# Kernel tuning notes

Measured on AMD Instinct MI355X. Metric: run time of the kernel, lower is better.

The kernel has to match this reference:

```python
import jax, jax.numpy as jnp
import numpy as np

EPS = 1e-5  # BatchNorm eps (torch default)

def _wq(w):
    # W8A16 fake-quant: per-output-channel symmetric int8 quantize + dequantize
    s = jnp.max(jnp.abs(w), axis=tuple(range(1, w.ndim)), keepdims=True) / 127.0
    s = jnp.maximum(s, 1e-8)
    q = jnp.clip(jnp.round(w / s), -128.0, 127.0)
    return q * s

def _conv(x, w, b, pad):
    y = jax.lax.conv_general_dilated(x, _wq(w), (1, 1), [(pad, pad), (pad, pad)],
                                     dimension_numbers=('NCHW', 'OIHW', 'NCHW'))
    return y + b[None, :, None, None]

def _bn(x, g, b, m, v):
    sh = (1, -1, 1, 1) if x.ndim == 4 else (1, -1)
    inv = jax.lax.rsqrt(v + EPS)
    return (x - m.reshape(sh)) * (inv * g).reshape(sh) + b.reshape(sh)

def _pool(x):
    return jax.lax.reduce_window(x, -jnp.inf, jax.lax.max, (1, 1, 2, 2), (1, 1, 2, 2), 'VALID')

def _ht(x):
    return jnp.clip(x, -1.0, 1.0)

def _linear(x, w, b):
    return x @ _wq(w).T + b

def setup_inputs() -> dict:
    key = jax.random.key(0)
    ks = iter(jax.random.split(key, 64))
    def rn(shape, s=0.05):
        return jax.random.normal(next(ks), shape, jnp.float32) * s
    d = {}
    d['x'] = jax.random.normal(next(ks), (1024, 1, 28, 28), jnp.float32)
    convs = [(1, 32, 5), (32, 64, 5), (64, 128, 3), (128, 256, 3), (256, 256, 1)]
    for i, (ci, co, k) in enumerate(convs, 1):
        d[f'w{i}'] = rn((co, ci, k, k), 0.1)
        d[f'b{i}'] = rn((co,))
        d[f'g{i}'] = jnp.ones((co,), jnp.float32)
        d[f'be{i}'] = jnp.zeros((co,), jnp.float32)
        d[f'mu{i}'] = rn((co,))
        d[f'va{i}'] = jax.random.uniform(next(ks), (co,), jnp.float32, 0.5, 1.5)
    fcs = [(2304, 1024), (1024, 512)]
    for i, (fi, fo) in enumerate(fcs, 1):
        d[f'fw{i}'] = rn((fo, fi), 0.05)
        d[f'fb{i}'] = rn((fo,))
        d[f'fg{i}'] = jnp.ones((fo,), jnp.float32)
        d[f'fbe{i}'] = jnp.zeros((fo,), jnp.float32)
        d[f'fmu{i}'] = rn((fo,))
        d[f'fva{i}'] = jax.random.uniform(next(ks), (fo,), jnp.float32, 0.5, 1.5)
    d['fw3'] = rn((10, 512), 0.05)
    d['fb3'] = rn((10,))
    return d

def reference(x, w1, b1, g1, be1, mu1, va1, w2, b2, g2, be2, mu2, va2,
              w3, b3, g3, be3, mu3, va3, w4, b4, g4, be4, mu4, va4,
              w5, b5, g5, be5, mu5, va5,
              fw1, fb1, fg1, fbe1, fmu1, fva1,
              fw2, fb2, fg2, fbe2, fmu2, fva2, fw3, fb3):
    h = _ht(_bn(_conv(x, w1, b1, 2), g1, be1, mu1, va1))                 # [B,32,28,28]
    h = _ht(_bn(_pool(_conv(h, w2, b2, 2)), g2, be2, mu2, va2))          # [B,64,14,14]
    h = _ht(_bn(_pool(_conv(h, w3, b3, 1)), g3, be3, mu3, va3))          # [B,128,7,7]
    h = _ht(_bn(_pool(_conv(h, w4, b4, 1)), g4, be4, mu4, va4))          # [B,256,3,3]
    h = _ht(_bn(_conv(h, w5, b5, 0), g5, be5, mu5, va5))                 # [B,256,3,3]
    h = h.reshape(h.shape[0], -1)                                        # [B,2304]
    h = _ht(_bn(_linear(h, fw1, fb1), fg1, fbe1, fmu1, fva1))            # [B,1024]
    h = _ht(_bn(_linear(h, fw2, fb2), fg2, fbe2, fmu2, fva2))            # [B,512]
    return _linear(h, fw3, fb3)                                          # [B,10]
```

## Files before the change

kernel.cpp:

```cpp
#include <hip/hip_runtime.h>
#include <hip/hip_bf16.h>
#include <math.h>


#define EPS 1e-5f

typedef __attribute__((ext_vector_type(8))) short bf16x8;
typedef __attribute__((ext_vector_type(4))) float f32x4;
typedef __attribute__((ext_vector_type(16))) float f32x16;
typedef __attribute__((ext_vector_type(4))) int i32x4;

__device__ __forceinline__ short f2bf(float f) {
  unsigned u = __builtin_bit_cast(unsigned, f);
  unsigned r = u + 0x7FFFu + ((u >> 16) & 1u);
  return (short)(r >> 16);
}
__device__ __forceinline__ float bf2f(short h) {
  unsigned u = ((unsigned)(unsigned short)h) << 16;
  return __builtin_bit_cast(float, u);
}
__device__ __forceinline__ int swz(int pin, int smask) {
  return (pin ^ (pin >> 2)) & smask;
}

struct QuantArgs {
  const float* w[8];
  float* q[8];
  float* sc[8];
  int cik[8];
  int cum[9];
};

__global__ __launch_bounds__(256) void quant_all(QuantArgs a) {
  int b = blockIdx.x;
  int t = 0;
  while (b >= a.cum[t + 1]) t++;
  int co = b - a.cum[t];
  int cik = a.cik[t];
  const float* src = a.w[t] + (size_t)co * cik;
  float m = 0.f;
  for (int i = threadIdx.x; i < cik; i += 256) m = fmaxf(m, fabsf(src[i]));
  #pragma unroll
  for (int o = 1; o < 64; o <<= 1) m = fmaxf(m, __shfl_xor(m, o));
  __shared__ float red[4];
  __shared__ float ssh;
  if ((threadIdx.x & 63) == 0) red[threadIdx.x >> 6] = m;
  __syncthreads();
  if (threadIdx.x == 0) {
    m = fmaxf(fmaxf(red[0], red[1]), fmaxf(red[2], red[3]));
    float s = fmaxf(m / 127.0f, 1e-8f);
    ssh = s;
    a.sc[t][co] = s;
  }
  __syncthreads();
  float s = ssh;
  float* dst = a.q[t];
  if (dst) {
    float* d = dst + (size_t)co * cik;
    for (int i = threadIdx.x; i < cik; i += 256) {
      float q = rintf(src[i] / s);
      q = fminf(fmaxf(q, -128.f), 127.f);
      d[i] = q * s;
    }
  }
}

__global__ __launch_bounds__(256) void repack_c1(const float* __restrict__ w,
                                                 const float* __restrict__ sc,
                                                 short* __restrict__ dst) {
  int i = blockIdx.x * 256 + threadIdx.x;
  if (i >= 1024) return;
  int oc = i >> 5, t = i & 31;
  float v = 0.f;
  if (t < 25) {
    float s = sc[oc];
    v = fminf(fmaxf(rintf(w[oc * 25 + t] / s), -128.f), 127.f);
  }
  dst[(((oc >> 4) * 4 + (t >> 3)) * 16 + (oc & 15)) * 8 + (t & 7)] = f2bf(v);
}

__global__ __launch_bounds__(256) void repack_frag(const float* __restrict__ w,
                                                   const float* __restrict__ sc,
                                                   short* __restrict__ dst,
                                                   int CO, int CI, int KK, int OCCH) {
  int i = blockIdx.x * 256 + threadIdx.x;
  int total = CO * CI * KK;
  if (i >= total) return;
  int oc = i / (CI * KK);
  int r = i - oc * (CI * KK);
  int ci = r / KK;
  int kk = r - ci * KK;
  float s = sc[oc];
  float q = fminf(fmaxf(rintf(w[i] / s), -128.f), 127.f);
  int NTC = OCCH >> 4;
  int KS = CI >> 5; if (KS == 0) KS = 1;
  int chunk = oc / OCCH;
  int ocl = oc - chunk * OCCH;
  int ntl = ocl >> 4, mr = ocl & 15;
  int ks = ci >> 5, qq = (ci >> 3) & 3, j = ci & 7;
  size_t d = ((((((size_t)(chunk * KK + kk) * NTC + ntl) * KS + ks) * 4 + qq) * 16 + mr)) * 8 + j;
  dst[d] = f2bf(q);
}

__global__ __launch_bounds__(256) void repack_frag32(const float* __restrict__ w,
                                                     const float* __restrict__ sc,
                                                     short* __restrict__ dst,
                                                     int CO, int CI, int KK, int OCCH) {
  int i = blockIdx.x * 256 + threadIdx.x;
  int total = CO * CI * KK;
  if (i >= total) return;
  int oc = i / (CI * KK);
  int r = i - oc * (CI * KK);
  int ci = r / KK;
  int kk = r - ci * KK;
  float s = sc[oc];
  float q = fminf(fmaxf(rintf(w[i] / s), -128.f), 127.f);
  int NT32 = OCCH >> 5;
  int KS16 = CI >> 4;
  int chunk = oc / OCCH;
  int ocl = oc - chunk * OCCH;
  int nt = ocl >> 5, n32 = ocl & 31;
  int ks = ci >> 4, hh = (ci >> 3) & 1, j = ci & 7;
  size_t d = ((((size_t)(chunk * KK + kk) * NT32 + nt) * KS16 + ks) * 64 + hh * 32 + n32) * 8 + j;
  dst[d] = f2bf(q);
}

__global__ __launch_bounds__(256) void repack_fc(const float* __restrict__ w,
                                                 const float* __restrict__ sc,
                                                 short* __restrict__ dst,
                                                 int K, int KC, int total) {
  int i = blockIdx.x * 256 + threadIdx.x;
  if (i >= total) return;
  int n = i / K, k = i - n * K;
  float s = sc[n];
  float q = fminf(fmaxf(rintf(w[i] / s), -128.f), 127.f);
  int nblk = n >> 6, ntl = (n >> 4) & 3, mr = n & 15;
  int kc = k >> 7, ks = (k >> 5) & 3, qq = (k >> 3) & 3, j = k & 7;
  size_t d = (((((((size_t)nblk * KC + kc) * 4 + ntl) * 4 + ks) * 4 + qq) * 16 + mr)) * 8 + j;
  dst[d] = f2bf(q);
}

__global__ __launch_bounds__(256) void transpose_w5(const float* __restrict__ src,
                                                    float* __restrict__ dst) {
  int i = blockIdx.x * 256 + threadIdx.x;
  int oc = i >> 8, ci = i & 255;
  dst[ci * 256 + oc] = src[i];
}

struct BnArgs {
  const float* p[7][5];
  const float* wsc;
  float* ab;
  int C[7];
  int abo[7];
  int sco[7];
  int us[7];
  int cum[8];
};

__global__ __launch_bounds__(256) void bn_all(BnArgs a) {
  int i = blockIdx.x * 256 + threadIdx.x;
  if (i >= a.cum[7]) return;
  int t = 0;
  while (i >= a.cum[t + 1]) t++;
  int c = i - a.cum[t];
  float A = a.p[t][1][c] / sqrtf(a.p[t][4][c] + EPS);
  float B = (a.p[t][0][c] - a.p[t][3][c]) * A + a.p[t][2][c];
  float As = a.us[t] ? A * a.wsc[a.sco[t] + c] : A;
  a.ab[a.abo[t] + c] = As;
  a.ab[a.abo[t] + a.C[t] + c] = B;
}

__global__ __launch_bounds__(448, 2) void conv1_mfma(
    const float* __restrict__ x, const short* __restrict__ wb1,
    const float* __restrict__ ab, short* __restrict__ out) {
  __shared__ __align__(16) float sx[784];
  __shared__ __align__(16) short sim[784 * 32];
  __shared__ __align__(16) short sw1[1024];
  const int tid = threadIdx.x;
  const int img = blockIdx.x;
  for (int i = tid; i < 784; i += 448) sx[i] = x[(size_t)img * 784 + i];
  for (int i = tid; i < 1024; i += 448) sw1[i] = wb1[i];
  __syncthreads();
  for (int i = tid; i < 25088; i += 448) {
    int p = i >> 5, t = i & 31;
    short v = 0;
    if (t < 25) {
      int py = p / 28, px = p - py * 28;
      int iy = py + t / 5 - 2, ix = px + t % 5 - 2;
      if ((unsigned)iy < 28u && (unsigned)ix < 28u) v = f2bf(sx[iy * 28 + ix]);
    }
    sim[i] = v;
  }
  __syncthreads();
  const int lane = tid & 63, wv = tid >> 6;
  const int mrow = lane & 15, quad = lane >> 4;
  f32x4 acc[7][2];
  #pragma unroll
  for (int i = 0; i < 7; ++i) {
    acc[i][0] = (f32x4){0.f, 0.f, 0.f, 0.f};
    acc[i][1] = (f32x4){0.f, 0.f, 0.f, 0.f};
  }
  #pragma unroll
  for (int i = 0; i < 7; ++i) {
    const int mt = wv * 7 + i;
    const bf16x8 a = *(const bf16x8*)&sim[(mt * 16 + mrow) * 32 + quad * 8];
    #pragma unroll
    for (int nt = 0; nt < 2; ++nt) {
      const bf16x8 b = *(const bf16x8*)&sw1[(nt * 4 + quad) * 128 + mrow * 8];
      acc[i][nt] = __builtin_amdgcn_mfma_f32_16x16x32_bf16(a, b, acc[i][nt], 0, 0, 0);
    }
  }
  #pragma unroll
  for (int i = 0; i < 7; ++i) {
    const int mt = wv * 7 + i;
    #pragma unroll
    for (int nt = 0; nt < 2; ++nt) {
      const int oc = nt * 16 + mrow;
      const float A = ab[oc], Bc = ab[32 + oc];
      #pragma unroll
      for (int r = 0; r < 4; ++r) {
        const int p = mt * 16 + quad * 4 + r;
        float v = fminf(fmaxf(acc[i][nt][r] * A + Bc, -1.f), 1.f);
        out[((size_t)img * 784 + p) * 32 + oc] = f2bf(v);
      }
    }
  }
}

template <int CIN, int COUT, int KW, int PAD, int IN_W, int PW, int IMGS,
          int TPI, int MTW, int OCCH, int TG>
__global__ __launch_bounds__(448, 2) void conv23_mfma32(
    const short* __restrict__ in, const short* __restrict__ wfrag,
    const float* __restrict__ ab, short* __restrict__ out) {
  constexpr int S = CIN / 8;
  constexpr int KS16 = CIN / 16;
  constexpr int NT32 = OCCH / 32;
  constexpr int NPIX = IN_W * IN_W;
  constexpr int PP = PW * PW;
  constexpr int KK = KW * KW;
  constexpr int CHUNKS = COUT / OCCH;
  constexpr int NGRP = KK / TG;
  constexpr int WG = TG * NT32 * KS16 * 512;
  constexpr int ITEMS = IMGS * TPI;
  constexpr int INCH = IMGS * NPIX * S;

  __shared__ __align__(16) short simg[IMGS * NPIX * CIN];
  __shared__ __align__(16) short sw[WG];
  __shared__ __align__(16) short zfrag[8];

  const int tid = threadIdx.x;
  const int img0 = blockIdx.x * IMGS;
  const int lane = tid & 63, wv = tid >> 6;
  const int l31 = lane & 31, h = lane >> 5;

  if (tid < 8) zfrag[tid] = 0;

  int yy[MTW], xx[MTW], ibs[MTW], lt_[MTW], il_[MTW];
  bool rv[MTW], uv[MTW];
  #pragma unroll
  for (int i = 0; i < MTW; ++i) {
    int u = wv + i * 7;
    uv[i] = u < ITEMS;
    int uu = uv[i] ? u : 0;
    int il = uu / TPI, lt = uu - il * TPI;
    int m = lt * 32 + l31;
    int pp = m >> 2, cd = m & 3;
    rv[i] = uv[i] && (pp < PP);
    int py = pp / PW, px = pp - py * PW;
    yy[i] = py * 2 + (cd >> 1);
    xx[i] = px * 2 + (cd & 1);
    ibs[i] = il * (NPIX * S);
    lt_[i] = lt; il_[i] = il;
  }

  {
    const i32x4* gsrc = (const i32x4*)(in + (size_t)img0 * NPIX * CIN);
    for (int c = tid; c < INCH; c += 448) {
      int il = c / (NPIX * S);
      int r = c - il * (NPIX * S);
      int pix = r / S;
      int blk = r & (S - 1);
      ((i32x4*)simg)[il * (NPIX * S) + pix * S + (blk ^ swz(pix, S - 1))] = gsrc[c];
    }
  }

  for (int ch = 0; ch < CHUNKS; ++ch) {
    f32x16 acc[MTW][NT32];
    #pragma unroll
    for (int i = 0; i < MTW; ++i)
      #pragma unroll
      for (int nt = 0; nt < NT32; ++nt)
        #pragma unroll
        for (int e = 0; e < 16; ++e) acc[i][nt][e] = 0.f;

    for (int tg = 0; tg < NGRP; ++tg) {
      __syncthreads();
      const i32x4* wsrc = (const i32x4*)(wfrag +
          ((size_t)ch * KK + tg * TG) * (NT32 * KS16 * 512));
      for (int u2 = tid; u2 < WG / 8; u2 += 448) ((i32x4*)sw)[u2] = wsrc[u2];
      __syncthreads();

      #pragma unroll
      for (int tt = 0; tt < TG; ++tt) {
        const int t = tg * TG + tt;
        const int dy = t / KW - PAD, dx = t % KW - PAD;
        int aoff[MTW], sx[MTW];
        #pragma unroll
        for (int i = 0; i < MTW; ++i) {
          int iy = yy[i] + dy, ix = xx[i] + dx;
          bool ok = rv[i] && ((unsigned)iy < (unsigned)IN_W) &&
                    ((unsigned)ix < (unsigned)IN_W);
          int pin = iy * IN_W + ix;
          aoff[i] = ok ? (ibs[i] + pin * S) * 8 : -1;
          sx[i] = swz(pin, S - 1);
        }
        #pragma unroll
        for (int ks = 0; ks < KS16; ++ks) {
          bf16x8 af[MTW];
          #pragma unroll
          for (int i = 0; i < MTW; ++i) {
            const short* p = (aoff[i] >= 0)
                ? &simg[aoff[i] + (((ks * 2 + h) ^ sx[i]) * 8)] : zfrag;
            af[i] = *(const bf16x8*)p;
          }
          #pragma unroll
          for (int nt = 0; nt < NT32; ++nt) {
            const bf16x8 bf = *(const bf16x8*)&sw[
                (((tt * NT32 + nt) * KS16 + ks) * 64 + lane) * 8];
            #pragma unroll
            for (int i = 0; i < MTW; ++i)
              acc[i][nt] = __builtin_amdgcn_mfma_f32_32x32x16_bf16(
                  af[i], bf, acc[i][nt], 0, 0, 0);
          }
        }
      }
    }

    #pragma unroll
    for (int i = 0; i < MTW; ++i) {
      #pragma unroll
      for (int nt = 0; nt < NT32; ++nt) {
        const int oc = ch * OCCH + nt * 32 + l31;
        const float A = ab[oc], Bc = ab[COUT + oc];
        #pragma unroll
        for (int g = 0; g < 4; ++g) {
          const int ppo = lt_[i] * 8 + 2 * g + h;
          if (uv[i] && ppo < PP) {
            float mx = fmaxf(fmaxf(acc[i][nt][g * 4 + 0], acc[i][nt][g * 4 + 1]),
                             fmaxf(acc[i][nt][g * 4 + 2], acc[i][nt][g * 4 + 3]));
            float v = fminf(fmaxf(mx * A + Bc, -1.f), 1.f);
            out[((size_t)(img0 + il_[i]) * PP + ppo) * COUT + oc] = f2bf(v);
          }
        }
      }
    }
  }
}

__global__ __launch_bounds__(512, 2) void conv4_mfma(
    const short* __restrict__ in,
    const short* __restrict__ wfrag,
    const float* __restrict__ ab, float* __restrict__ out) {
  constexpr int S = 16, NPIX = 49, PP = 9;
  __shared__ __align__(16) short simg[2 * NPIX * 128];
  __shared__ __align__(16) short swb[2][32768];
  const int tid = threadIdx.x;
  const int img0 = blockIdx.x * 2;
  const int lane = tid & 63, wv = tid >> 6;
  const int mrow = lane & 15, quad = lane >> 4;

  {
    const i32x4* gsrc = (const i32x4*)(in + (size_t)img0 * NPIX * 128);
    for (int c = tid; c < 2 * NPIX * S; c += 512) {
      int il = c / (NPIX * S);
      int r = c - il * (NPIX * S);
      int pix = r >> 4, blk = r & 15;
      ((i32x4*)simg)[il * NPIX * S + pix * S + (blk ^ (pix & 15))] = gsrc[c];
    }
    for (int u = tid; u < 4096; u += 512)
      ((i32x4*)swb[0])[u] = ((const i32x4*)wfrag)[u];
  }

  int yy[6], xx[6], ibs[6], ppo_[6], ilv[6];
  bool rv[6], pv[6];
  #pragma unroll
  for (int i = 0; i < 6; ++i) {
    int il = i / 3, lt = i - il * 3;
    int m = lt * 16 + mrow;
    int pp = m >> 2, cd = m & 3;
    rv[i] = pp < PP;
    int py = pp / 3, px = pp - py * 3;
    yy[i] = py * 2 + (cd >> 1);
    xx[i] = px * 2 + (cd & 1);
    ibs[i] = il * NPIX * S;
    ilv[i] = il;
    ppo_[i] = lt * 4 + quad;
    pv[i] = ppo_[i] < PP;
  }
  const int nt0 = wv, nt1 = wv + 8;
  f32x4 acc[6][2];
  #pragma unroll
  for (int i = 0; i < 6; ++i) {
    acc[i][0] = (f32x4){0.f, 0.f, 0.f, 0.f};
    acc[i][1] = (f32x4){0.f, 0.f, 0.f, 0.f};
  }
  __syncthreads();

  int dy = -1, dx = -1;
  for (int t = 0; t < 9; ++t) {
    const int buf = t & 1;
    if (t < 8) {
      const i32x4* wsrc = (const i32x4*)(wfrag + (size_t)(t + 1) * 32768);
      for (int u = tid; u < 4096; u += 512) ((i32x4*)swb[buf ^ 1])[u] = wsrc[u];
    }
    #pragma unroll
    for (int ks = 0; ks < 4; ++ks) {
      bf16x8 af[6];
      #pragma unroll
      for (int i = 0; i < 6; ++i) {
        int iy = yy[i] + dy, ix = xx[i] + dx;
        bool ok = rv[i] && (unsigned)iy < 7u && (unsigned)ix < 7u;
        int pin = iy * 7 + ix;
        int blk = (ks * 4 + quad) ^ (pin & 15);
        af[i] = ok ? *(const bf16x8*)&simg[(ibs[i] + pin * S + blk) * 8]
                   : (bf16x8){0, 0, 0, 0, 0, 0, 0, 0};
      }
      const bf16x8 b0 = *(const bf16x8*)&swb[buf][((nt0 * 4 + ks) * 4 + quad) * 128 + mrow * 8];
      const bf16x8 b1 = *(const bf16x8*)&swb[buf][((nt1 * 4 + ks) * 4 + quad) * 128 + mrow * 8];
      #pragma unroll
      for (int i = 0; i < 6; ++i) {
        acc[i][0] = __builtin_amdgcn_mfma_f32_16x16x32_bf16(af[i], b0, acc[i][0], 0, 0, 0);
        acc[i][1] = __builtin_amdgcn_mfma_f32_16x16x32_bf16(af[i], b1, acc[i][1], 0, 0, 0);
      }
    }
    dx++;
    if (dx == 2) { dx = -1; dy++; }
    __syncthreads();
  }

  #pragma unroll
  for (int i = 0; i < 6; ++i) {
    if (pv[i]) {
      #pragma unroll
      for (int nj = 0; nj < 2; ++nj) {
        const int oc = (nj ? nt1 : nt0) * 16 + mrow;
        const f32x4 a = acc[i][nj];
        float mx = fmaxf(fmaxf(a[0], a[1]), fmaxf(a[2], a[3]));
        float v = fminf(fmaxf(mx * ab[oc] + ab[256 + oc], -1.f), 1.f);
        out[((size_t)(img0 + ilv[i]) * PP + ppo_[i]) * 256 + oc] = v;
      }
    }
  }
}

__global__ __launch_bounds__(256, 2) void conv5_fc(
    const float* __restrict__ in, const float* __restrict__ w5t,
    const float* __restrict__ ab, short* __restrict__ oh, short* __restrict__ ol) {
  __shared__ float sin[9 * 256];
  const int img = blockIdx.x;
  const int oc = threadIdx.x;
  for (int i = threadIdx.x; i < 2304; i += 256)
    sin[i] = in[(size_t)img * 2304 + i];
  __syncthreads();
  float acc[9];
  #pragma unroll
  for (int p = 0; p < 9; ++p) acc[p] = 0.f;
  for (int ci = 0; ci < 256; ++ci) {
    const float wv = w5t[ci * 256 + oc];
    #pragma unroll
    for (int p = 0; p < 9; ++p) acc[p] += sin[p * 256 + ci] * wv;
  }
  const float A = ab[oc], Bc = ab[256 + oc];
  const int mblk = img >> 6, mtq = (img >> 4) & 3, mr = img & 15;
  #pragma unroll
  for (int p = 0; p < 9; ++p) {
    float v = fminf(fmaxf(acc[p] * A + Bc, -1.f), 1.f);
    int k = oc * 9 + p;
    int kc = k >> 7, ks = (k >> 5) & 3, qq = (k >> 3) & 3, j = k & 7;
    size_t d = (((((((size_t)mblk * 18 + kc) * 4 + mtq) * 4 + ks) * 4 + qq) * 16 + mr)) * 8 + j;
    short hi = f2bf(v);
    oh[d] = hi;
    ol[d] = f2bf(v - bf2f(hi));
  }
}

template <int KC, int OUTMODE, int KC2, int NALL>
__global__ __launch_bounds__(256, 2) void fc_mfma(
    const short* __restrict__ Xh, const short* __restrict__ Xl,
    const short* __restrict__ Wf, const float* __restrict__ ab,
    float* __restrict__ outF, short* __restrict__ outH, short* __restrict__ outL) {
  __shared__ __align__(16) short sxh[8192];
  __shared__ __align__(16) short sxl[8192];
  __shared__ __align__(16) short swt[8192];
  const int tid = threadIdx.x;
  const int bn = blockIdx.x, bm = blockIdx.y;
  const int lane = tid & 63, wv = tid >> 6;
  const int mrow = lane & 15, quad = lane >> 4;
  f32x4 acc[4];
  #pragma unroll
  for (int nt = 0; nt < 4; ++nt) acc[nt] = (f32x4){0.f, 0.f, 0.f, 0.f};
  for (int kc = 0; kc < KC; ++kc) {
    __syncthreads();
    {
      const size_t xo = ((size_t)bm * KC + kc) * 8192;
      const size_t wo = ((size_t)bn * KC + kc) * 8192;
      #pragma unroll
      for (int u = 0; u < 4; ++u) {
        ((i32x4*)sxh)[tid + u * 256] = ((const i32x4*)(Xh + xo))[tid + u * 256];
        ((i32x4*)sxl)[tid + u * 256] = ((const i32x4*)(Xl + xo))[tid + u * 256];
        ((i32x4*)swt)[tid + u * 256] = ((const i32x4*)(Wf + wo))[tid + u * 256];
      }
    }
    __syncthreads();
    #pragma unroll
    for (int ks = 0; ks < 4; ++ks) {
      const int ao = (((wv * 4 + ks) * 4 + quad) * 16 + mrow) * 8;
      const bf16x8 ah = *(const bf16x8*)&sxh[ao];
      const bf16x8 al = *(const bf16x8*)&sxl[ao];
      #pragma unroll
      for (int nt = 0; nt < 4; ++nt) {
        const bf16x8 b = *(const bf16x8*)&swt[(((nt * 4 + ks) * 4 + quad) * 16 + mrow) * 8];
        acc[nt] = __builtin_amdgcn_mfma_f32_16x16x32_bf16(ah, b, acc[nt], 0, 0, 0);
        acc[nt] = __builtin_amdgcn_mfma_f32_16x16x32_bf16(al, b, acc[nt], 0, 0, 0);
      }
    }
  }
  #pragma unroll
  for (int nt = 0; nt < 4; ++nt) {
    const int n = bn * 64 + nt * 16 + mrow;
    const float A = ab[n], Bc = ab[NALL + n];
    #pragma unroll
    for (int r = 0; r < 4; ++r) {
      const int m = bm * 64 + wv * 16 + quad * 4 + r;
      float v = fminf(fmaxf(acc[nt][r] * A + Bc, -1.f), 1.f);
      if (OUTMODE == 0) {
        size_t d = (((((((size_t)(m >> 6) * KC2 + (n >> 7)) * 4 + ((m >> 4) & 3)) * 4 +
                       ((n >> 5) & 3)) * 4 + ((n >> 3) & 3)) * 16 + (m & 15))) * 8 + (n & 7);
        short hi = f2bf(v);
        outH[d] = hi;
        outL[d] = f2bf(v - bf2f(hi));
      } else {
        outF[(size_t)m * NALL + n] = v;
      }
    }
  }
}

__global__ __launch_bounds__(256) void fc3_kernel(
    const float* __restrict__ X, const float* __restrict__ W,
    const float* __restrict__ bias, float* __restrict__ out) {
  __shared__ float ws[512 * 10 + 16];
  for (int li = threadIdx.x; li < 5120; li += 256) {
    int n = li / 512, k = li - n * 512;
    ws[k * 10 + n] = W[li];
  }
  __syncthreads();
  const int il = threadIdx.x >> 4, n = threadIdx.x & 15;
  const int img = blockIdx.x * 16 + il;
  if (n < 10) {
    const float* xp = X + (size_t)img * 512;
    float s = 0.f;
    for (int k = 0; k < 512; ++k) s += xp[k] * ws[k * 10 + n];
    out[img * 10 + n] = s + bias[n];
  }
}

extern "C" void kernel_launch(void* const* d_in, const int* in_sizes, int n_in,
                              void* d_out, int out_size, void* d_ws, size_t ws_size,
                              hipStream_t stream) {
  (void)in_sizes; (void)n_in; (void)out_size; (void)ws_size;
  const float* x = (const float*)d_in[0];
  float* W = (float*)d_ws;

  float* wsc  = W + 0;
  float* ab   = W + 2304;
  float* qs5  = W + 6912;
  float* fq3  = W + 72448;
  short* wb1  = (short*)(W + 77568);
  short* wb2  = (short*)(W + 78080);
  short* wb3  = (short*)(W + 103680);
  short* wb4  = (short*)(W + 140544);
  float* w5t  = W + 288000;
  short* fqb1 = (short*)(W + 353536);
  short* fqb2 = (short*)(W + 1533184);
  short* h1   = (short*)(W + 1795328);
  short* h2   = (short*)(W + 14640384);
  short* h3   = (short*)(W + 21062912);
  float* h4   = W + 24274176;
  short* h5h  = (short*)(W + 26633472);
  short* h5l  = (short*)(W + 27813120);
  short* f1h  = (short*)(W + 28992768);
  short* f1l  = (short*)(W + 29517056);
  float* f2   = W + 30041344;

  QuantArgs qa;
  const int widx[8] = {1, 7, 13, 19, 25, 31, 37, 43};
  float* qdst[8] = {nullptr, nullptr, nullptr, nullptr, qs5, nullptr, nullptr, fq3};
  const int sco8[8] = {0, 32, 96, 224, 480, 736, 1760, 2272};
  const int cik[8] = {25, 800, 576, 1152, 256, 2304, 1024, 512};
  const int co[8] = {32, 64, 128, 256, 256, 1024, 512, 10};
  int cum = 0;
  for (int i = 0; i < 8; ++i) {
    qa.w[i] = (const float*)d_in[widx[i]];
    qa.q[i] = qdst[i];
    qa.sc[i] = wsc + sco8[i];
    qa.cik[i] = cik[i];
    qa.cum[i] = cum;
    cum += co[i];
  }
  qa.cum[8] = cum;
  hipLaunchKernelGGL(quant_all, dim3(cum), dim3(256), 0, stream, qa);

  hipLaunchKernelGGL(repack_c1, dim3(4), dim3(256), 0, stream,
                     (const float*)d_in[1], wsc + 0, wb1);
  hipLaunchKernelGGL(repack_frag32, dim3(200), dim3(256), 0, stream,
                     (const float*)d_in[7], wsc + 32, wb2, 64, 32, 25, 64);
  hipLaunchKernelGGL(repack_frag32, dim3(288), dim3(256), 0, stream,
                     (const float*)d_in[13], wsc + 96, wb3, 128, 64, 9, 64);
  hipLaunchKernelGGL(repack_frag, dim3(1152), dim3(256), 0, stream,
                     (const float*)d_in[19], wsc + 224, wb4, 256, 128, 9, 256);
  hipLaunchKernelGGL(repack_fc, dim3(9216), dim3(256), 0, stream,
                     (const float*)d_in[31], wsc + 736, fqb1, 2304, 18, 1024 * 2304);
  hipLaunchKernelGGL(repack_fc, dim3(2048), dim3(256), 0, stream,
                     (const float*)d_in[37], wsc + 1760, fqb2, 1024, 8, 512 * 1024);
  hipLaunchKernelGGL(transpose_w5, dim3(256), dim3(256), 0, stream, qs5, w5t);

  BnArgs ba;
  const int bbase[7] = {2, 8, 14, 20, 26, 32, 38};
  const int bc[7] = {32, 64, 128, 256, 256, 1024, 512};
  const int abo[7] = {0, 64, 192, 448, 960, 1472, 3520};
  const int us7[7] = {1, 1, 1, 1, 0, 1, 1};
  int bcum = 0;
  for (int t = 0; t < 7; ++t) {
    for (int j = 0; j < 5; ++j) ba.p[t][j] = (const float*)d_in[bbase[t] + j];
    ba.C[t] = bc[t];
    ba.abo[t] = abo[t];
    ba.sco[t] = sco8[t];
    ba.us[t] = us7[t];
    ba.cum[t] = bcum;
    bcum += bc[t];
  }
  ba.cum[7] = bcum;
  ba.ab = ab;
  ba.wsc = wsc;
  hipLaunchKernelGGL(bn_all, dim3((bcum + 255) / 256), dim3(256), 0, stream, ba);

  hipLaunchKernelGGL(conv1_mfma, dim3(1024), dim3(448), 0, stream,
                     x, wb1, ab + 0, h1);
  hipLaunchKernelGGL((conv23_mfma32<32, 64, 5, 2, 28, 14, 1, 25, 4, 64, 5>),
                     dim3(1024), dim3(448), 0, stream, h1, wb2, ab + 64, h2);
  hipLaunchKernelGGL((conv23_mfma32<64, 128, 3, 1, 14, 7, 2, 7, 2, 64, 3>),
                     dim3(512), dim3(448), 0, stream, h2, wb3, ab + 192, h3);
  hipLaunchKernelGGL(conv4_mfma, dim3(512), dim3(512), 0, stream,
                     h3, wb4, ab + 448, h4);
  hipLaunchKernelGGL(conv5_fc, dim3(1024), dim3(256), 0, stream,
                     h4, w5t, ab + 960, h5h, h5l);

  hipLaunchKernelGGL((fc_mfma<18, 0, 8, 1024>), dim3(16, 16), dim3(256), 0, stream,
                     h5h, h5l, fqb1, ab + 1472, nullptr, f1h, f1l);
  hipLaunchKernelGGL((fc_mfma<8, 1, 0, 512>), dim3(8, 16), dim3(256), 0, stream,
                     f1h, f1l, fqb2, ab + 3520, f2, nullptr, nullptr);
  hipLaunchKernelGGL(fc3_kernel, dim3(64), dim3(256), 0, stream,
                     f2, fq3, (const float*)d_in[44], (float*)d_out);
}
```

Measured before the change: 475.3 us.

## Fuse weight prep, split conv2 per half-image, run conv5 as MFMA GEMM

Merges the weight quantize and all repack kernels into one prep_all launch that writes the MFMA fragment layouts directly. conv2 gets a dedicated kernel that splits each image into two halves (2048 blocks of 256 threads), and conv3 moves to 4-wave blocks. conv4 now writes hi/lo bf16 fragments, so the 1x1 conv5 runs through the fc_mfma GEMM path instead of a scalar FP32 kernel. The aim is fewer launches, more parallelism for conv2, and tensor-core use for conv5, at the cost of some redundant halo loads and a new output mode in the GEMM.

```diff
diff --git a/kernel.cpp b/kernel.cpp
--- a/kernel.cpp
+++ b/kernel.cpp
@@ -22,22 +22,32 @@
 __device__ __forceinline__ int swz(int pin, int smask) {
   return (pin ^ (pin >> 2)) & smask;
 }
-
-struct QuantArgs {
+__device__ __forceinline__ float qclip(float w, float s) {
+  return fminf(fmaxf(rintf(w / s), -128.f), 127.f);
+}
+
+struct PrepArgs {
   const float* w[8];
-  float* q[8];
-  float* sc[8];
+  short* dsth[8];
+  float* dstf;
+  float* sc;
+  int sco[8];
   int cik[8];
+  int kind[8];
+  int KK[8];
+  int CI[8];
+  int OCCH[8];
+  int KC[8];
   int cum[9];
 };
 
-__global__ __launch_bounds__(256) void quant_all(QuantArgs a) {
+__global__ __launch_bounds__(256) void prep_all(PrepArgs a) {
   int b = blockIdx.x;
   int t = 0;
   while (b >= a.cum[t + 1]) t++;
-  int co = b - a.cum[t];
+  int oc = b - a.cum[t];
   int cik = a.cik[t];
-  const float* src = a.w[t] + (size_t)co * cik;
+  const float* src = a.w[t] + (size_t)oc * cik;
   float m = 0.f;
   for (int i = threadIdx.x; i < cik; i += 256) m = fmaxf(m, fabsf(src[i]));
   #pragma unroll
@@ -50,101 +60,56 @@
     m = fmaxf(fmaxf(red[0], red[1]), fmaxf(red[2], red[3]));
     float s = fmaxf(m / 127.0f, 1e-8f);
     ssh = s;
-    a.sc[t][co] = s;
+    a.sc[a.sco[t] + oc] = s;
   }
   __syncthreads();
-  float s = ssh;
-  float* dst = a.q[t];
-  if (dst) {
-    float* d = dst + (size_t)co * cik;
-    for (int i = threadIdx.x; i < cik; i += 256) {
-      float q = rintf(src[i] / s);
-      q = fminf(fmaxf(q, -128.f), 127.f);
-      d[i] = q * s;
-    }
-  }
-}
-
-__global__ __launch_bounds__(256) void repack_c1(const float* __restrict__ w,
-                                                 const float* __restrict__ sc,
-                                                 short* __restrict__ dst) {
-  int i = blockIdx.x * 256 + threadIdx.x;
-  if (i >= 1024) return;
-  int oc = i >> 5, t = i & 31;
-  float v = 0.f;
-  if (t < 25) {
-    float s = sc[oc];
-    v = fminf(fmaxf(rintf(w[oc * 25 + t] / s), -128.f), 127.f);
-  }
-  dst[(((oc >> 4) * 4 + (t >> 3)) * 16 + (oc & 15)) * 8 + (t & 7)] = f2bf(v);
-}
-
-__global__ __launch_bounds__(256) void repack_frag(const float* __restrict__ w,
-                                                   const float* __restrict__ sc,
-                                                   short* __restrict__ dst,
-                                                   int CO, int CI, int KK, int OCCH) {
-  int i = blockIdx.x * 256 + threadIdx.x;
-  int total = CO * CI * KK;
-  if (i >= total) return;
-  int oc = i / (CI * KK);
-  int r = i - oc * (CI * KK);
-  int ci = r / KK;
-  int kk = r - ci * KK;
-  float s = sc[oc];
-  float q = fminf(fmaxf(rintf(w[i] / s), -128.f), 127.f);
-  int NTC = OCCH >> 4;
-  int KS = CI >> 5; if (KS == 0) KS = 1;
-  int chunk = oc / OCCH;
-  int ocl = oc - chunk * OCCH;
-  int ntl = ocl >> 4, mr = ocl & 15;
-  int ks = ci >> 5, qq = (ci >> 3) & 3, j = ci & 7;
-  size_t d = ((((((size_t)(chunk * KK + kk) * NTC + ntl) * KS + ks) * 4 + qq) * 16 + mr)) * 8 + j;
-  dst[d] = f2bf(q);
-}
-
-__global__ __launch_bounds__(256) void repack_frag32(const float* __restrict__ w,
-                                                     const float* __restrict__ sc,
-                                                     short* __restrict__ dst,
-                                                     int CO, int CI, int KK, int OCCH) {
-  int i = blockIdx.x * 256 + threadIdx.x;
-  int total = CO * CI * KK;
-  if (i >= total) return;
-  int oc = i / (CI * KK);
-  int r = i - oc * (CI * KK);
-  int ci = r / KK;
-  int kk = r - ci * KK;
-  float s = sc[oc];
-  float q = fminf(fmaxf(rintf(w[i] / s), -128.f), 127.f);
-  int NT32 = OCCH >> 5;
-  int KS16 = CI >> 4;
-  int chunk = oc / OCCH;
-  int ocl = oc - chunk * OCCH;
-  int nt = ocl >> 5, n32 = ocl & 31;
-  int ks = ci >> 4, hh = (ci >> 3) & 1, j = ci & 7;
-  size_t d = ((((size_t)(chunk * KK + kk) * NT32 + nt) * KS16 + ks) * 64 + hh * 32 + n32) * 8 + j;
-  dst[d] = f2bf(q);
-}
-
-__global__ __launch_bounds__(256) void repack_fc(const float* __restrict__ w,
-                                                 const float* __restrict__ sc,
-                                                 short* __restrict__ dst,
-                                                 int K, int KC, int total) {
-  int i = blockIdx.x * 256 + threadIdx.x;
-  if (i >= total) return;
-  int n = i / K, k = i - n * K;
-  float s = sc[n];
-  float q = fminf(fmaxf(rintf(w[i] / s), -128.f), 127.f);
-  int nblk = n >> 6, ntl = (n >> 4) & 3, mr = n & 15;
-  int kc = k >> 7, ks = (k >> 5) & 3, qq = (k >> 3) & 3, j = k & 7;
-  size_t d = (((((((size_t)nblk * KC + kc) * 4 + ntl) * 4 + ks) * 4 + qq) * 16 + mr)) * 8 + j;
-  dst[d] = f2bf(q);
-}
-
-__global__ __launch_bounds__(256) void transpose_w5(const float* __restrict__ src,
-                                                    float* __restrict__ dst) {
-  int i = blockIdx.x * 256 + threadIdx.x;
-  int oc = i >> 8, ci = i & 255;
-  dst[ci * 256 + oc] = src[i];
+  const float s = ssh;
+  const int kind = a.kind[t];
+  short* dst = a.dsth[t];
+  if (kind == 0) {
+    for (int tt = threadIdx.x; tt < 32; tt += 256) {
+      float q = (tt < 25) ? qclip(src[tt], s) : 0.f;
+      dst[(((oc >> 4) * 4 + (tt >> 3)) * 16 + (oc & 15)) * 8 + (tt & 7)] = f2bf(q);
+    }
+  } else if (kind == 1) {
+    const int KK = a.KK[t], CI = a.CI[t], OCCH = a.OCCH[t];
+    const int NT32 = OCCH >> 5, KS16 = CI >> 4;
+    const int chunk = oc / OCCH, ocl = oc - chunk * OCCH;
+    const int nt = ocl >> 5, n32 = ocl & 31;
+    for (int idx = threadIdx.x; idx < cik; idx += 256) {
+      int ci = idx / KK, kk = idx - ci * KK;
+      float q = qclip(src[idx], s);
+      int ks = ci >> 4, hh = (ci >> 3) & 1, j = ci & 7;
+      size_t d = ((((size_t)(chunk * KK + kk) * NT32 + nt) * KS16 + ks) * 64 +
+                  hh * 32 + n32) * 8 + j;
+      dst[d] = f2bf(q);
+    }
+  } else if (kind == 2) {
+    const int KK = a.KK[t], CI = a.CI[t], OCCH = a.OCCH[t];
+    const int NTC = OCCH >> 4, KS = CI >> 5;
+    const int chunk = oc / OCCH, ocl = oc - chunk * OCCH;
+    const int ntl = ocl >> 4, mr = ocl & 15;
+    for (int idx = threadIdx.x; idx < cik; idx += 256) {
+      int ci = idx / KK, kk = idx - ci * KK;
+      float q = qclip(src[idx], s);
+      int ks = ci >> 5, qq = (ci >> 3) & 3, j = ci & 7;
+      size_t d = ((((((size_t)(chunk * KK + kk) * NTC + ntl) * KS + ks) * 4 + qq) *
+                   16 + mr)) * 8 + j;
+      dst[d] = f2bf(q);
+    }
+  } else if (kind == 3) {
+    const int KC = a.KC[t];
+    const int nblk = oc >> 6, ntl = (oc >> 4) & 3, mr = oc & 15;
+    for (int k = threadIdx.x; k < cik; k += 256) {
+      float q = qclip(src[k], s);
+      size_t d = ((((((size_t)nblk * KC + (k >> 7)) * 4 + ntl) * 4 + ((k >> 5) & 3)) *
+                   4 + ((k >> 3) & 3)) * 16 + mr) * 8 + (k & 7);
+      dst[d] = f2bf(q);
+    }
+  } else {
+    for (int k = threadIdx.x; k < cik; k += 256)
+      a.dstf[(size_t)oc * cik + k] = qclip(src[k], s) * s;
+  }
 }
 
 struct BnArgs {
@@ -154,7 +119,6 @@
   int C[7];
   int abo[7];
   int sco[7];
-  int us[7];
   int cum[8];
 };
 
@@ -166,8 +130,7 @@
   int c = i - a.cum[t];
   float A = a.p[t][1][c] / sqrtf(a.p[t][4][c] + EPS);
   float B = (a.p[t][0][c] - a.p[t][3][c]) * A + a.p[t][2][c];
-  float As = a.us[t] ? A * a.wsc[a.sco[t] + c] : A;
-  a.ab[a.abo[t] + c] = As;
+  a.ab[a.abo[t] + c] = A * a.wsc[a.sco[t] + c];
   a.ab[a.abo[t] + a.C[t] + c] = B;
 }
 
@@ -228,9 +191,114 @@
   }
 }
 
+__global__ __launch_bounds__(256, 2) void conv2_half(
+    const short* __restrict__ in, const short* __restrict__ wfrag,
+    const float* __restrict__ ab, short* __restrict__ out) {
+  constexpr int S = 4;
+  __shared__ __align__(16) short simg[18 * 28 * 32];
+  __shared__ __align__(16) short sw[5 * 2048];
+  __shared__ __align__(16) short zfrag[8];
+  const int tid = threadIdx.x;
+  const int img = blockIdx.x >> 1, half = blockIdx.x & 1;
+  const int lane = tid & 63, wv = tid >> 6;
+  const int l31 = lane & 31, h = lane >> 5;
+  if (tid < 8) zfrag[tid] = 0;
+
+  {
+    const i32x4* gin = (const i32x4*)(in + ((size_t)img * 784 + half * 12 * 28) * 32);
+    const int lyb = half ? 0 : 2;
+    for (int c = tid; c < 1792; c += 256) {
+      int ps = c >> 2, blk = c & 3;
+      int pin_l = (lyb + ps / 28) * 28 + ps % 28;
+      ((i32x4*)simg)[pin_l * S + (blk ^ swz(pin_l, 3))] = gin[c];
+    }
+  }
+
+  int ygl[4], yll[4], xx[4], ppb[4];
+  bool uv[4], rv[4];
+  #pragma unroll
+  for (int i = 0; i < 4; ++i) {
+    int u = wv + i * 4;
+    uv[i] = u < 13;
+    int m = u * 32 + l31;
+    int ppl = m >> 2, cd = m & 3;
+    rv[i] = uv[i] && (ppl < 98);
+    int pr = ppl / 14, pc = ppl - pr * 14;
+    ygl[i] = (half * 7 + pr) * 2 + (cd >> 1);
+    yll[i] = ygl[i] - (half * 14 - 2);
+    xx[i] = pc * 2 + (cd & 1);
+    ppb[i] = u * 8;
+  }
+
+  f32x16 acc[4][2];
+  #pragma unroll
+  for (int i = 0; i < 4; ++i)
+    #pragma unroll
+    for (int nt = 0; nt < 2; ++nt)
+      #pragma unroll
+      for (int e = 0; e < 16; ++e) acc[i][nt][e] = 0.f;
+
+  for (int tg = 0; tg < 5; ++tg) {
+    __syncthreads();
+    const i32x4* wsrc = (const i32x4*)(wfrag + tg * 5 * 2048);
+    for (int u2 = tid; u2 < 1280; u2 += 256) ((i32x4*)sw)[u2] = wsrc[u2];
+    __syncthreads();
+    #pragma unroll
+    for (int tt = 0; tt < 5; ++tt) {
+      const int t = tg * 5 + tt;
+      const int dy = t / 5 - 2, dx = t % 5 - 2;
+      int aoff[4], sxh[4];
+      #pragma unroll
+      for (int i = 0; i < 4; ++i) {
+        int iy = ygl[i] + dy, ix = xx[i] + dx;
+        bool ok = rv[i] && ((unsigned)iy < 28u) && ((unsigned)ix < 28u);
+        int pin_l = (yll[i] + dy) * 28 + ix;
+        aoff[i] = ok ? pin_l * (S * 8) : -1;
+        sxh[i] = swz(pin_l, 3);
+      }
+      #pragma unroll
+      for (int ks = 0; ks < 2; ++ks) {
+        bf16x8 af[4];
+        #pragma unroll
+        for (int i = 0; i < 4; ++i) {
+          const short* p = (aoff[i] >= 0)
+              ? &simg[aoff[i] + (((ks * 2 + h) ^ sxh[i]) * 8)] : zfrag;
+          af[i] = *(const bf16x8*)p;
+        }
+        #pragma unroll
+        for (int nt = 0; nt < 2; ++nt) {
+          const bf16x8 bf = *(const bf16x8*)&sw[(((tt * 2 + nt) * 2 + ks) * 64 + lane) * 8];
+          #pragma unroll
+          for (int i = 0; i < 4; ++i)
+            acc[i][nt] = __builtin_amdgcn_mfma_f32_32x32x16_bf16(af[i], bf, acc[i][nt], 0, 0, 0);
+        }
+      }
+    }
+  }
+
+  #pragma unroll
+  for (int i = 0; i < 4; ++i) {
+    #pragma unroll
+    for (int nt = 0; nt < 2; ++nt) {
+      const int oc = nt * 32 + l31;
+      const float A = ab[oc], Bc = ab[64 + oc];
+      #pragma unroll
+      for (int g = 0; g < 4; ++g) {
+        const int ppo = ppb[i] + 2 * g + h;
+        if (uv[i] && ppo < 98) {
+          float mx = fmaxf(fmaxf(acc[i][nt][g * 4 + 0], acc[i][nt][g * 4 + 1]),
+                           fmaxf(acc[i][nt][g * 4 + 2], acc[i][nt][g * 4 + 3]));
+          float v = fminf(fmaxf(mx * A + Bc, -1.f), 1.f);
+          out[((size_t)img * 196 + half * 98 + ppo) * 64 + oc] = f2bf(v);
+        }
+      }
+    }
+  }
+}
+
 template <int CIN, int COUT, int KW, int PAD, int IN_W, int PW, int IMGS,
-          int TPI, int MTW, int OCCH, int TG>
-__global__ __launch_bounds__(448, 2) void conv23_mfma32(
+          int TPI, int MTW, int OCCH, int TG, int WAVES>
+__global__ __launch_bounds__(256, 2) void conv23_mfma32(
     const short* __restrict__ in, const short* __restrict__ wfrag,
     const float* __restrict__ ab, short* __restrict__ out) {
   constexpr int S = CIN / 8;
@@ -260,7 +328,7 @@
   bool rv[MTW], uv[MTW];
   #pragma unroll
   for (int i = 0; i < MTW; ++i) {
-    int u = wv + i * 7;
+    int u = wv + i * WAVES;
     uv[i] = u < ITEMS;
     int uu = uv[i] ? u : 0;
     int il = uu / TPI, lt = uu - il * TPI;
@@ -276,7 +344,7 @@
 
   {
     const i32x4* gsrc = (const i32x4*)(in + (size_t)img0 * NPIX * CIN);
-    for (int c = tid; c < INCH; c += 448) {
+    for (int c = tid; c < INCH; c += 256) {
       int il = c / (NPIX * S);
       int r = c - il * (NPIX * S);
       int pix = r / S;
@@ -298,14 +366,14 @@
       __syncthreads();
       const i32x4* wsrc = (const i32x4*)(wfrag +
           ((size_t)ch * KK + tg * TG) * (NT32 * KS16 * 512));
-      for (int u2 = tid; u2 < WG / 8; u2 += 448) ((i32x4*)sw)[u2] = wsrc[u2];
+      for (int u2 = tid; u2 < WG / 8; u2 += 256) ((i32x4*)sw)[u2] = wsrc[u2];
       __syncthreads();
 
       #pragma unroll
       for (int tt = 0; tt < TG; ++tt) {
         const int t = tg * TG + tt;
         const int dy = t / KW - PAD, dx = t % KW - PAD;
-        int aoff[MTW], sx[MTW];
+        int aoff[MTW], sxh[MTW];
         #pragma unroll
         for (int i = 0; i < MTW; ++i) {
           int iy = yy[i] + dy, ix = xx[i] + dx;
@@ -313,7 +381,7 @@
                     ((unsigned)ix < (unsigned)IN_W);
           int pin = iy * IN_W + ix;
           aoff[i] = ok ? (ibs[i] + pin * S) * 8 : -1;
-          sx[i] = swz(pin, S - 1);
+          sxh[i] = swz(pin, S - 1);
         }
         #pragma unroll
         for (int ks = 0; ks < KS16; ++ks) {
@@ -321,7 +389,7 @@
           #pragma unroll
           for (int i = 0; i < MTW; ++i) {
             const short* p = (aoff[i] >= 0)
-                ? &simg[aoff[i] + (((ks * 2 + h) ^ sx[i]) * 8)] : zfrag;
+                ? &simg[aoff[i] + (((ks * 2 + h) ^ sxh[i]) * 8)] : zfrag;
             af[i] = *(const bf16x8*)p;
           }
           #pragma unroll
@@ -361,7 +429,8 @@
 __global__ __launch_bounds__(512, 2) void conv4_mfma(
     const short* __restrict__ in,
     const short* __restrict__ wfrag,
-    const float* __restrict__ ab, float* __restrict__ out) {
+    const float* __restrict__ ab,
+    short* __restrict__ outH, short* __restrict__ outL) {
   constexpr int S = 16, NPIX = 49, PP = 9;
   __shared__ __align__(16) short simg[2 * NPIX * 128];
   __shared__ __align__(16) short swb[2][32768];
@@ -448,40 +517,14 @@
         const f32x4 a = acc[i][nj];
         float mx = fmaxf(fmaxf(a[0], a[1]), fmaxf(a[2], a[3]));
         float v = fminf(fmaxf(mx * ab[oc] + ab[256 + oc], -1.f), 1.f);
-        out[((size_t)(img0 + ilv[i]) * PP + ppo_[i]) * 256 + oc] = v;
-      }
-    }
-  }
-}
-
-__global__ __launch_bounds__(256, 2) void conv5_fc(
-    const float* __restrict__ in, const float* __restrict__ w5t,
-    const float* __restrict__ ab, short* __restrict__ oh, short* __restrict__ ol) {
-  __shared__ float sin[9 * 256];
-  const int img = blockIdx.x;
-  const int oc = threadIdx.x;
-  for (int i = threadIdx.x; i < 2304; i += 256)
-    sin[i] = in[(size_t)img * 2304 + i];
-  __syncthreads();
-  float acc[9];
-  #pragma unroll
-  for (int p = 0; p < 9; ++p) acc[p] = 0.f;
-  for (int ci = 0; ci < 256; ++ci) {
-    const float wv = w5t[ci * 256 + oc];
-    #pragma unroll
-    for (int p = 0; p < 9; ++p) acc[p] += sin[p * 256 + ci] * wv;
-  }
-  const float A = ab[oc], Bc = ab[256 + oc];
-  const int mblk = img >> 6, mtq = (img >> 4) & 3, mr = img & 15;
-  #pragma unroll
-  for (int p = 0; p < 9; ++p) {
-    float v = fminf(fmaxf(acc[p] * A + Bc, -1.f), 1.f);
-    int k = oc * 9 + p;
-    int kc = k >> 7, ks = (k >> 5) & 3, qq = (k >> 3) & 3, j = k & 7;
-    size_t d = (((((((size_t)mblk * 18 + kc) * 4 + mtq) * 4 + ks) * 4 + qq) * 16 + mr)) * 8 + j;
-    short hi = f2bf(v);
-    oh[d] = hi;
-    ol[d] = f2bf(v - bf2f(hi));
+        const int m5 = (img0 + ilv[i]) * 9 + ppo_[i];
+        size_t d = ((((((size_t)(m5 >> 6) * 2 + (oc >> 7)) * 4 + ((m5 >> 4) & 3)) * 4 +
+                     ((oc >> 5) & 3)) * 4 + ((oc >> 3) & 3)) * 16 + (m5 & 15)) * 8 + (oc & 7);
+        short hi = f2bf(v);
+        outH[d] = hi;
+        outL[d] = f2bf(v - bf2f(hi));
+      }
+    }
   }
 }
 
@@ -540,8 +583,16 @@
         short hi = f2bf(v);
         outH[d] = hi;
         outL[d] = f2bf(v - bf2f(hi));
+      } else if (OUTMODE == 1) {
+        outF[(size_t)m * NALL + n] = v;
       } else {
-        outF[(size_t)m * NALL + n] = v;
+        const int imgq = m / 9, p = m - imgq * 9;
+        const int k1 = n * 9 + p;
+        size_t d = ((((((size_t)(imgq >> 6) * KC2 + (k1 >> 7)) * 4 + ((imgq >> 4) & 3)) * 4 +
+                     ((k1 >> 5) & 3)) * 4 + ((k1 >> 3) & 3)) * 16 + (imgq & 15)) * 8 + (k1 & 7);
+        short hi = f2bf(v);
+        outH[d] = hi;
+        outL[d] = f2bf(v - bf2f(hi));
       }
     }
   }
@@ -575,69 +626,65 @@
 
   float* wsc  = W + 0;
   float* ab   = W + 2304;
-  float* qs5  = W + 6912;
-  float* fq3  = W + 72448;
-  short* wb1  = (short*)(W + 77568);
-  short* wb2  = (short*)(W + 78080);
-  short* wb3  = (short*)(W + 103680);
-  short* wb4  = (short*)(W + 140544);
-  float* w5t  = W + 288000;
-  short* fqb1 = (short*)(W + 353536);
-  short* fqb2 = (short*)(W + 1533184);
-  short* h1   = (short*)(W + 1795328);
-  short* h2   = (short*)(W + 14640384);
-  short* h3   = (short*)(W + 21062912);
-  float* h4   = W + 24274176;
-  short* h5h  = (short*)(W + 26633472);
-  short* h5l  = (short*)(W + 27813120);
-  short* f1h  = (short*)(W + 28992768);
-  short* f1l  = (short*)(W + 29517056);
-  float* f2   = W + 30041344;
-
-  QuantArgs qa;
+  float* fq3  = W + 6912;
+  short* wb1  = (short*)(W + 12032);
+  short* wb2  = (short*)(W + 12544);
+  short* wb3  = (short*)(W + 38144);
+  short* wb4  = (short*)(W + 75008);
+  short* wb5  = (short*)(W + 222464);
+  short* fqb1 = (short*)(W + 255232);
+  short* fqb2 = (short*)(W + 1434880);
+  short* h1   = (short*)(W + 1697024);
+  short* h2   = (short*)(W + 14542080);
+  short* h3   = (short*)(W + 20964608);
+  short* h4h  = (short*)(W + 24175872);
+  short* h4l  = (short*)(W + 25355520);
+  short* h5h  = (short*)(W + 26535168);
+  short* h5l  = (short*)(W + 27714816);
+  short* f1h  = (short*)(W + 28894464);
+  short* f1l  = (short*)(W + 29418752);
+  float* f2   = W + 29943040;
+
+  PrepArgs pa;
   const int widx[8] = {1, 7, 13, 19, 25, 31, 37, 43};
-  float* qdst[8] = {nullptr, nullptr, nullptr, nullptr, qs5, nullptr, nullptr, fq3};
+  short* pdst[8] = {wb1, wb2, wb3, wb4, wb5, fqb1, fqb2, nullptr};
   const int sco8[8] = {0, 32, 96, 224, 480, 736, 1760, 2272};
-  const int cik[8] = {25, 800, 576, 1152, 256, 2304, 1024, 512};
-  const int co[8] = {32, 64, 128, 256, 256, 1024, 512, 10};
+  const int cik8[8] = {25, 800, 576, 1152, 256, 2304, 1024, 512};
+  const int co8[8] = {32, 64, 128, 256, 256, 1024, 512, 10};
+  const int kind8[8] = {0, 1, 1, 2, 3, 3, 3, 4};
+  const int KK8[8] = {25, 25, 9, 9, 1, 1, 1, 1};
+  const int CI8[8] = {1, 32, 64, 128, 256, 2304, 1024, 512};
+  const int OCCH8[8] = {32, 64, 64, 256, 256, 1024, 512, 10};
+  const int KC8[8] = {1, 1, 1, 1, 2, 18, 8, 1};
   int cum = 0;
   for (int i = 0; i < 8; ++i) {
-    qa.w[i] = (const float*)d_in[widx[i]];
-    qa.q[i] = qdst[i];
-    qa.sc[i] = wsc + sco8[i];
-    qa.cik[i] = cik[i];
-    qa.cum[i] = cum;
-    cum += co[i];
-  }
-  qa.cum[8] = cum;
-  hipLaunchKernelGGL(quant_all, dim3(cum), dim3(256), 0, stream, qa);
-
-  hipLaunchKernelGGL(repack_c1, dim3(4), dim3(256), 0, stream,
-                     (const float*)d_in[1], wsc + 0, wb1);
-  hipLaunchKernelGGL(repack_frag32, dim3(200), dim3(256), 0, stream,
-                     (const float*)d_in[7], wsc + 32, wb2, 64, 32, 25, 64);
-  hipLaunchKernelGGL(repack_frag32, dim3(288), dim3(256), 0, stream,
-                     (const float*)d_in[13], wsc + 96, wb3, 128, 64, 9, 64);
-  hipLaunchKernelGGL(repack_frag, dim3(1152), dim3(256), 0, stream,
-                     (const float*)d_in[19], wsc + 224, wb4, 256, 128, 9, 256);
-  hipLaunchKernelGGL(repack_fc, dim3(9216), dim3(256), 0, stream,
-                     (const float*)d_in[31], wsc + 736, fqb1, 2304, 18, 1024 * 2304);
-  hipLaunchKernelGGL(repack_fc, dim3(2048), dim3(256), 0, stream,
-                     (const float*)d_in[37], wsc + 1760, fqb2, 1024, 8, 512 * 1024);
-  hipLaunchKernelGGL(transpose_w5, dim3(256), dim3(256), 0, stream, qs5, w5t);
+    pa.w[i] = (const float*)d_in[widx[i]];
+    pa.dsth[i] = pdst[i];
+    pa.sco[i] = sco8[i];
+    pa.cik[i] = cik8[i];
+    pa.kind[i] = kind8[i];
+    pa.KK[i] = KK8[i];
+    pa.CI[i] = CI8[i];
+    pa.OCCH[i] = OCCH8[i];
+    pa.KC[i] = KC8[i];
+    pa.cum[i] = cum;
+    cum += co8[i];
+  }
+  pa.cum[8] = cum;
+  pa.dstf = fq3;
+  pa.sc = wsc;
+  hipLaunchKernelGGL(prep_all, dim3(cum), dim3(256), 0, stream, pa);
 
   BnArgs ba;
   const int bbase[7] = {2, 8, 14, 20, 26, 32, 38};
   const int bc[7] = {32, 64, 128, 256, 256, 1024, 512};
   const int abo[7] = {0, 64, 192, 448, 960, 1472, 3520};
-  const int us7[7] = {1, 1, 1, 1, 0, 1, 1};
   int bcum = 0;
   for (int t = 0; t < 7; ++t) {
     for (int j = 0; j < 5; ++j) ba.p[t][j] = (const float*)d_in[bbase[t] + j];
     ba.C[t] = bc[t];
     ba.abo[t] = abo[t];
     ba.sco[t] = sco8[t];
-    ba.us[t] = us7[t];
     ba.cum[t] = bcum;
     bcum += bc[t];
   }
@@ -648,14 +695,14 @@
 
   hipLaunchKernelGGL(conv1_mfma, dim3(1024), dim3(448), 0, stream,
                      x, wb1, ab + 0, h1);
-  hipLaunchKernelGGL((conv23_mfma32<32, 64, 5, 2, 28, 14, 1, 25, 4, 64, 5>),
-                     dim3(1024), dim3(448), 0, stream, h1, wb2, ab + 64, h2);
-  hipLaunchKernelGGL((conv23_mfma32<64, 128, 3, 1, 14, 7, 2, 7, 2, 64, 3>),
-                     dim3(512), dim3(448), 0, stream, h2, wb3, ab + 192, h3);
+  hipLaunchKernelGGL(conv2_half, dim3(2048), dim3(256), 0, stream,
+                     h1, wb2, ab + 64, h2);
+  hipLaunchKernelGGL((conv23_mfma32<64, 128, 3, 1, 14, 7, 2, 7, 4, 64, 3, 4>),
+                     dim3(512), dim3(256), 0, stream, h2, wb3, ab + 192, h3);
   hipLaunchKernelGGL(conv4_mfma, dim3(512), dim3(512), 0, stream,
-                     h3, wb4, ab + 448, h4);
-  hipLaunchKernelGGL(conv5_fc, dim3(1024), dim3(256), 0, stream,
-                     h4, w5t, ab + 960, h5h, h5l);
+                     h3, wb4, ab + 448, h4h, h4l);
+  hipLaunchKernelGGL((fc_mfma<2, 2, 18, 256>), dim3(4, 144), dim3(256), 0, stream,
+                     h4h, h4l, wb5, ab + 960, nullptr, h5h, h5l);
 
   hipLaunchKernelGGL((fc_mfma<18, 0, 8, 1024>), dim3(16, 16), dim3(256), 0, stream,
                      h5h, h5l, fqb1, ab + 1472, nullptr, f1h, f1l);
```

After: 436.6 us. 8.1% less time.
